# Kernel optimization log

Measured on AMD Instinct MI355X. Metric: run time of the kernel, lower is better.

The kernel has to match this reference:

```python
import jax, jax.numpy as jnp
import numpy as np

N_HEAD = 8
D_MODEL = 128  # per-head dim == d_model in this 'interpretable' MHA
B, S = 2, 2048
LN_EPS = 1e-3  # keras LayerNormalization default epsilon


def setup_inputs() -> dict:
    key = jax.random.key(0)
    ks = jax.random.split(key, 8)
    sc = 1.0 / np.sqrt(D_MODEL)
    q = jax.random.normal(ks[0], (B, S, D_MODEL), jnp.float32)
    k = jax.random.normal(ks[1], (B, S, D_MODEL), jnp.float32)
    v = jax.random.normal(ks[2], (B, S, D_MODEL), jnp.float32)
    # multiplicative causal mask (lower-triangular ones), broadcast over B,H
    mask = jnp.tril(jnp.ones((S, S), jnp.float32))[None, None, :, :]
    Wq = jax.random.normal(ks[3], (D_MODEL, N_HEAD * D_MODEL), jnp.float32) * sc
    Wk = jax.random.normal(ks[4], (D_MODEL, N_HEAD * D_MODEL), jnp.float32) * sc
    Wv = jax.random.normal(ks[5], (D_MODEL, N_HEAD * D_MODEL), jnp.float32) * sc
    Wo = jax.random.normal(ks[6], (N_HEAD * D_MODEL, D_MODEL), jnp.float32) * sc
    gamma = jnp.ones((D_MODEL,), jnp.float32)
    beta = jnp.zeros((D_MODEL,), jnp.float32)
    return {"q": q, "k": k, "v": v, "mask": mask, "Wq": Wq, "Wk": Wk,
            "Wv": Wv, "Wo": Wo, "gamma": gamma, "beta": beta}


def reference(q, k, v, mask, Wq, Wk, Wv, Wo, gamma, beta):
    b = q.shape[0]
    # projections -> [B, H, S, D]
    def split_heads(x):
        return x.reshape(b, -1, N_HEAD, D_MODEL).transpose(0, 2, 1, 3)
    qs = split_heads(q @ Wq)
    ks_ = split_heads(k @ Wk)
    vs = split_heads(v @ Wv)
    scores = jnp.einsum('bhqd,bhkd->bhqk', qs, ks_) / jnp.sqrt(jnp.float32(D_MODEL))
    scores = scores * mask  # multiplicative mask (NOT additive -inf)
    attn = jax.nn.softmax(scores, axis=-1)
    # dropout layers are identity at inference
    out = jnp.einsum('bhqk,bhkd->bhqd', attn, vs)
    out = out.transpose(0, 2, 1, 3).reshape(b, -1, N_HEAD * D_MODEL)
    out = out @ Wo
    # keras LayerNorm (axis=-1, eps=1e-3)
    mu = jnp.mean(out, axis=-1, keepdims=True)
    var = jnp.var(out, axis=-1, keepdims=True)
    out = (out - mu) * jax.lax.rsqrt(var + LN_EPS) * gamma + beta
    return out
```

## Files before the change

### kernel.cpp

```cpp
#include <hip/hip_runtime.h>
#include <math.h>

#define B 2
#define S 2048
#define H 8
#define D 128
#define DM 1024
#define BH 16

typedef unsigned short u16;
typedef __attribute__((ext_vector_type(8))) short bf16x8;
typedef __attribute__((ext_vector_type(8))) unsigned short u16x8;
typedef __attribute__((ext_vector_type(4))) float f32x4;

__device__ __forceinline__ float bf2f(u16 x) {
    union { unsigned u; float f; } c; c.u = ((unsigned)x) << 16; return c.f;
}
__device__ __forceinline__ u16 f2bf(float f) {
    union { unsigned u; float f; } c; c.f = f;
    unsigned u = c.u; u += 0x7fffu + ((u >> 16) & 1u);
    return (u16)(u >> 16);
}
__device__ __forceinline__ u16 ftr(float f) {
    union { unsigned u; float f; } c; c.f = f;
    return (u16)(c.u >> 16);
}

#define MFMA16(a, b, c) __builtin_amdgcn_mfma_f32_16x16x32_bf16((a), (b), (c), 0, 0, 0)

__device__ __forceinline__ void gload_lds16(const void* g, void* l) {
    __builtin_amdgcn_global_load_lds(
        (__attribute__((address_space(1))) void*)(unsigned long long)(g),
        (__attribute__((address_space(3))) void*)(unsigned long long)(l), 16, 0, 0);
}

__global__ __launch_bounds__(256) void prep_kernel(
    const float* __restrict__ Wq, const float* __restrict__ Wk, const float* __restrict__ Wv,
    const float* __restrict__ Wo, u16* __restrict__ WT, u16* __restrict__ WoT)
{
    __shared__ __align__(16) u16 Wl[128][132];
    int tid = threadIdx.x, by = blockIdx.x;
    if (by < 16) {
        int k0 = by * 64;
#pragma unroll
        for (int i = 0; i < 8; i++) {
            int e = i * 256 + tid; int kk = e >> 5, n4 = e & 31;
            float4 w4 = *(const float4*)&Wo[(size_t)(k0 + kk) * D + n4 * 4];
            ushort4 p; p.x = ftr(w4.x); p.y = ftr(w4.y); p.z = ftr(w4.z); p.w = ftr(w4.w);
            *(ushort4*)&Wl[kk][n4 * 4] = p;
        }
        __syncthreads();
#pragma unroll
        for (int i = 0; i < 4; i++) {
            int e = i * 256 + tid; int n = e >> 3, ko = e & 7;
            u16x8 g;
#pragma unroll
            for (int j = 0; j < 8; j++) g[j] = Wl[ko * 8 + j][n];
            *(u16x8*)&WoT[(size_t)n * DM + k0 + ko * 8] = g;
        }
    } else {
        int tile = by - 16;
        int t = tile >> 3, h = tile & 7;
        const float* W = (t == 0) ? Wq : (t == 1) ? Wk : Wv;
        int col0 = h * 128;
#pragma unroll
        for (int i = 0; i < 16; i++) {
            int e = i * 256 + tid; int kk = e >> 5, n4 = e & 31;
            float4 w4 = *(const float4*)&W[(size_t)kk * DM + col0 + n4 * 4];
            ushort4 p; p.x = ftr(w4.x); p.y = ftr(w4.y); p.z = ftr(w4.z); p.w = ftr(w4.w);
            *(ushort4*)&Wl[kk][n4 * 4] = p;
        }
        __syncthreads();
        u16* WTt = WT + (size_t)tile * (128 * 128);
#pragma unroll
        for (int i = 0; i < 8; i++) {
            int e = i * 256 + tid; int n = e >> 4, ko = e & 15;
            u16x8 g;
#pragma unroll
            for (int j = 0; j < 8; j++) g[j] = Wl[ko * 8 + j][n];
            *(u16x8*)&WTt[(size_t)n * 128 + ko * 8] = g;
        }
    }
}

__global__ __launch_bounds__(256) void proj_kernel(
    const float* __restrict__ q, const float* __restrict__ k, const float* __restrict__ v,
    const u16* __restrict__ WT,
    u16* __restrict__ Qo, u16* __restrict__ Ko, u16* __restrict__ VTo,
    float* __restrict__ Csum)
{
    __shared__ __align__(16) u16 Xs[64][136];
    __shared__ __align__(16) u16 Ws[128][136];
    int tid = threadIdx.x;
    int m0 = blockIdx.x * 64;
    int by = blockIdx.y;
    int t = by >> 3;
    int h = by & 7;
    const float* X = (t == 0) ? q : (t == 1) ? k : v;
    const u16* WTt = WT + (size_t)(t * 8 + h) * (128 * 128);

#pragma unroll
    for (int i = 0; i < 8; i++) {
        int e = i * 256 + tid; int r = e >> 5, c4 = e & 31;
        float4 x4 = *(const float4*)&X[(size_t)(m0 + r) * D + c4 * 4];
        ushort4 p; p.x = ftr(x4.x); p.y = ftr(x4.y); p.z = ftr(x4.z); p.w = ftr(x4.w);
        *(ushort4*)&Xs[r][c4 * 4] = p;
    }
#pragma unroll
    for (int i = 0; i < 8; i++) {
        int e = i * 256 + tid; int n = e >> 4, c8 = e & 15;
        *(u16x8*)&Ws[n][c8 * 8] = *(const u16x8*)&WTt[(size_t)n * 128 + c8 * 8];
    }
    __syncthreads();

    int w = tid >> 6, lane = tid & 63, quad = lane >> 4, ln = lane & 15;
    bf16x8 aX[4];
#pragma unroll
    for (int ks = 0; ks < 4; ks++)
        aX[ks] = *(const bf16x8*)&Xs[w * 16 + ln][ks * 32 + quad * 8];

    f32x4 zero = {0.f, 0.f, 0.f, 0.f};
    f32x4 acc[8];
#pragma unroll
    for (int nt = 0; nt < 8; nt++) acc[nt] = zero;

#pragma unroll
    for (int ks = 0; ks < 4; ks++) {
        bf16x8 bW[8];
#pragma unroll
        for (int nt = 0; nt < 8; nt++)
            bW[nt] = *(const bf16x8*)&Ws[nt * 16 + ln][ks * 32 + quad * 8];
#pragma unroll
        for (int nt = 0; nt < 8; nt++)
            acc[nt] = MFMA16(aX[ks], bW[nt], acc[nt]);
    }

    int bb = m0 >> 11, ss0 = m0 & 2047;
    int bh = bb * 8 + h;
    __syncthreads();
    if (t < 2) {
        u16 (*Ct)[136] = Xs;
        u16* O = (t == 0) ? Qo : Ko;
#pragma unroll
        for (int nt = 0; nt < 8; nt++)
#pragma unroll
            for (int r = 0; r < 4; r++)
                Ct[w * 16 + quad * 4 + r][nt * 16 + ln] = f2bf(acc[nt][r]);
        __syncthreads();
#pragma unroll
        for (int i = 0; i < 4; i++) {
            int e = i * 256 + tid; int r = e >> 4, c8 = e & 15;
            *(u16x8*)&O[((size_t)bh * S + ss0 + r) * D + c8 * 8] = *(const u16x8*)&Ct[r][c8 * 8];
        }
    } else {
        u16 (*Ct)[68] = (u16 (*)[68])&Xs[0][0];
#pragma unroll
        for (int nt = 0; nt < 8; nt++)
#pragma unroll
            for (int r = 0; r < 4; r++)
                Ct[nt * 16 + ln][w * 16 + quad * 4 + r] = f2bf(acc[nt][r]);
        __syncthreads();
#pragma unroll
        for (int i = 0; i < 4; i++) {
            int e = i * 256 + tid; int dloc = e >> 3, c8 = e & 7;
            *(u16x8*)&VTo[((size_t)bh * D + dloc) * S + ss0 + c8 * 8] =
                *(const u16x8*)&Ct[dloc][c8 * 8];
        }
        if (tid < 128) {
            int d = tid;
            float s = 0.f;
#pragma unroll
            for (int i = 0; i < 8; i++) {
                u16x8 v8 = *(const u16x8*)&Ct[d][i * 8];
#pragma unroll
                for (int j = 0; j < 8; j++) s += bf2f(v8[j]);
            }
            Csum[((size_t)bh * 32 + (ss0 >> 6)) * D + d] = s;
        }
    }
}

__global__ __launch_bounds__(256, 2) void attn_kernel(
    const u16* __restrict__ Qb, const u16* __restrict__ Kb, const u16* __restrict__ VTg,
    const float* __restrict__ Csum, u16* __restrict__ HOb)
{
    __shared__ __align__(16) u16 Ks[2][64][128];
    __shared__ __align__(16) u16 Vt[128][64];
    __shared__ __align__(16) u16 Ps[64][68];
    __shared__ float Lred[4][64];

    int tid = threadIdx.x;
    int bh = blockIdx.x;
    int y  = blockIdx.y;
    int qb = 31 - y;
    int q0 = qb * 64;
    int ntile = qb + 1;
    int w = tid >> 6, lane = tid & 63, quad = lane >> 4, ln = lane & 15;
    const u16* Qp  = Qb  + (size_t)bh * S * D;
    const u16* Kp  = Kb  + (size_t)bh * S * D;
    const u16* VTp = VTg + (size_t)bh * D * S;

#pragma unroll
    for (int i = 0; i < 4; i++) {
        int ci = i * 256 + tid;
        int r = ci >> 4, c = ci & 15;
        int sc = c ^ (r & 7);
        gload_lds16(&Qp[(size_t)(q0 + r) * D + sc * 8], (u16*)&Ks[1][0][0] + ci * 8);
    }
#pragma unroll
    for (int i = 0; i < 4; i++) {
        int ci = i * 256 + tid;
        int r = ci >> 4, c = ci & 15;
        int sc = c ^ (r & 7);
        gload_lds16(&Kp[(size_t)r * D + sc * 8], (u16*)&Ks[0][0][0] + ci * 8);
    }
    asm volatile("s_waitcnt vmcnt(4)" ::: "memory");
    __builtin_amdgcn_sched_barrier(0);
    __builtin_amdgcn_s_barrier();
    bf16x8 aQ[4][4];
#pragma unroll
    for (int rf = 0; rf < 4; rf++)
#pragma unroll
        for (int ks = 0; ks < 4; ks++) {
            int R = rf * 16 + ln;
            aQ[rf][ks] = *(const bf16x8*)&Ks[1][R][((ks * 4 + quad) ^ (R & 7)) * 8];
        }
    asm volatile("s_waitcnt vmcnt(0) lgkmcnt(0)" ::: "memory");
    __builtin_amdgcn_sched_barrier(0);
    __builtin_amdgcn_s_barrier();
#pragma unroll
    for (int i = 0; i < 4; i++) {
        int ci = i * 256 + tid;
        int dd = ci >> 3, c = ci & 7;
        int sc = c ^ (dd & 7);
        gload_lds16(&VTp[(size_t)dd * S + sc * 8], (u16*)&Vt[0][0] + ci * 8);
    }

    f32x4 zero = {0.f, 0.f, 0.f, 0.f};
    f32x4 accPV[4][2], acc_l[4];
#pragma unroll
    for (int rf = 0; rf < 4; rf++) { accPV[rf][0] = zero; accPV[rf][1] = zero; acc_l[rf] = zero; }
    bf16x8 bOnes;
#pragma unroll
    for (int j = 0; j < 8; j++) bOnes[j] = (short)0x3F80;
    const float scale = 0.08838834764831845f;

    for (int kt = 0; kt < ntile; kt++) {
        int cur = kt & 1, nxt = cur ^ 1;
        int k0 = kt * 64;
        bool pf = (kt + 1 < ntile);
        if (pf) {
#pragma unroll
            for (int i = 0; i < 4; i++) {
                int ci = i * 256 + tid;
                int r = ci >> 4, c = ci & 15;
                int sc = c ^ (r & 7);
                gload_lds16(&Kp[(size_t)(k0 + 64 + r) * D + sc * 8],
                            (u16*)&Ks[nxt][0][0] + ci * 8);
            }
        }
        f32x4 s[4];
#pragma unroll
        for (int rf = 0; rf < 4; rf++) s[rf] = zero;
        __builtin_amdgcn_s_setprio(1);
#pragma unroll
        for (int ks = 0; ks < 4; ks++) {
            int R = w * 16 + ln;
            bf16x8 bK = *(const bf16x8*)&Ks[cur][R][((ks * 4 + quad) ^ (R & 7)) * 8];
#pragma unroll
            for (int rf = 0; rf < 4; rf++)
                s[rf] = MFMA16(aQ[rf][ks], bK, s[rf]);
        }
        __builtin_amdgcn_s_setprio(0);
        int colb = k0 + w * 16 + ln;
#pragma unroll
        for (int rf = 0; rf < 4; rf++) {
            int rowb = q0 + rf * 16 + quad * 4;
#pragma unroll
            for (int r = 0; r < 4; r++) {
                float tv = (colb <= rowb + r) ? s[rf][r] : 0.f;
                Ps[rf * 16 + quad * 4 + r][w * 16 + ln] = f2bf(__expf(tv * scale));
            }
        }
        if (pf) asm volatile("s_waitcnt vmcnt(4) lgkmcnt(0)" ::: "memory");
        else    asm volatile("s_waitcnt vmcnt(0) lgkmcnt(0)" ::: "memory");
        __builtin_amdgcn_sched_barrier(0);
        __builtin_amdgcn_s_barrier();
        __builtin_amdgcn_s_setprio(1);
#pragma unroll
        for (int ks = 0; ks < 2; ks++) {
            bf16x8 aP[4];
#pragma unroll
            for (int rf = 0; rf < 4; rf++)
                aP[rf] = *(const bf16x8*)&Ps[rf * 16 + ln][ks * 32 + quad * 8];
            int rv0 = w * 32 + ln, rv1 = w * 32 + 16 + ln;
            bf16x8 v0 = *(const bf16x8*)&Vt[rv0][((ks * 4 + quad) ^ (rv0 & 7)) * 8];
            bf16x8 v1 = *(const bf16x8*)&Vt[rv1][((ks * 4 + quad) ^ (rv1 & 7)) * 8];
            if (((kt * 2 + ks) & 3) == w) {
#pragma unroll
                for (int rf = 0; rf < 4; rf++) acc_l[rf] = MFMA16(aP[rf], bOnes, acc_l[rf]);
            }
#pragma unroll
            for (int rf = 0; rf < 4; rf++) {
                accPV[rf][0] = MFMA16(aP[rf], v0, accPV[rf][0]);
                accPV[rf][1] = MFMA16(aP[rf], v1, accPV[rf][1]);
            }
        }
        __builtin_amdgcn_s_setprio(0);
        asm volatile("s_waitcnt vmcnt(0) lgkmcnt(0)" ::: "memory");
        __builtin_amdgcn_sched_barrier(0);
        __builtin_amdgcn_s_barrier();
        if (pf) {
#pragma unroll
            for (int i = 0; i < 4; i++) {
                int ci = i * 256 + tid;
                int dd = ci >> 3, c = ci & 7;
                int sc = c ^ (dd & 7);
                gload_lds16(&VTp[(size_t)dd * S + k0 + 64 + sc * 8], (u16*)&Vt[0][0] + ci * 8);
            }
        }
    }

    __syncthreads();
    if (ln == 0) {
#pragma unroll
        for (int rf = 0; rf < 4; rf++)
#pragma unroll
            for (int r = 0; r < 4; r++)
                Lred[w][rf * 16 + quad * 4 + r] = acc_l[rf][r];
    }
    __syncthreads();

    float suf0 = 0.f, suf1 = 0.f;
    for (int c = 31; c >= ntile; c--) {
        const float* cp = &Csum[((size_t)(bh * 32 + c)) * D + w * 32];
        suf0 += cp[ln];
        suf1 += cp[16 + ln];
    }
    int scount = S - ntile * 64;
    int b = bh >> 3, h = bh & 7;
#pragma unroll
    for (int rf = 0; rf < 4; rf++)
#pragma unroll
        for (int r = 0; r < 4; r++) {
            int row = rf * 16 + quad * 4 + r;
            int srow = q0 + row;
            float l = Lred[0][row] + Lred[1][row] + Lred[2][row] + Lred[3][row]
                      + (float)scount;
            float inv = 1.f / l;
            size_t base = ((size_t)(b * S + srow)) * DM + h * D + w * 32;
            HOb[base + ln]      = f2bf((accPV[rf][0][r] + suf0) * inv);
            HOb[base + 16 + ln] = f2bf((accPV[rf][1][r] + suf1) * inv);
        }
}

__global__ __launch_bounds__(256) void out_ln_kernel(
    const u16* __restrict__ HOb, const u16* __restrict__ WoT,
    const float* __restrict__ gamma, const float* __restrict__ beta,
    float* __restrict__ out)
{
    __shared__ __align__(16) u16 HOs[16][1048];
    __shared__ float Cs[16][132];
    int tid = threadIdx.x;
    int m0 = blockIdx.x * 16;
    int w = tid >> 6, lane = tid & 63, quad = lane >> 4, ln = lane & 15;
#pragma unroll
    for (int i = 0; i < 8; i++) {
        int e = i * 256 + tid; int r = e >> 7, c8 = e & 127;
        *(u16x8*)&HOs[r][c8 * 8] = *(const u16x8*)&HOb[(size_t)(m0 + r) * DM + c8 * 8];
    }
    __syncthreads();
    f32x4 zero = {0.f, 0.f, 0.f, 0.f};
    f32x4 acc[2] = {zero, zero};
#pragma unroll 4
    for (int ks = 0; ks < 32; ks++) {
        bf16x8 aH = *(const bf16x8*)&HOs[ln][ks * 32 + quad * 8];
        bf16x8 w0 = *(const bf16x8*)&WoT[(size_t)(w * 32 + ln) * DM + ks * 32 + quad * 8];
        bf16x8 w1 = *(const bf16x8*)&WoT[(size_t)(w * 32 + 16 + ln) * DM + ks * 32 + quad * 8];
        acc[0] = MFMA16(aH, w0, acc[0]);
        acc[1] = MFMA16(aH, w1, acc[1]);
    }
#pragma unroll
    for (int ct = 0; ct < 2; ct++)
#pragma unroll
        for (int r = 0; r < 4; r++)
            Cs[quad * 4 + r][w * 32 + ct * 16 + ln] = acc[ct][r];
    __syncthreads();

    int row = tid >> 4, t16 = tid & 15;
    float xv[8], sum = 0.f, sq = 0.f;
#pragma unroll
    for (int j = 0; j < 8; j++) {
        float x = Cs[row][t16 * 8 + j];
        xv[j] = x; sum += x; sq += x * x;
    }
#pragma unroll
    for (int off = 1; off < 16; off <<= 1) {
        sum += __shfl_xor(sum, off);
        sq  += __shfl_xor(sq, off);
    }
    float mu = sum * (1.f / 128.f);
    float var = sq * (1.f / 128.f) - mu * mu;
    float rstd = rsqrtf(var + 1e-3f);
    float o[8];
#pragma unroll
    for (int j = 0; j < 8; j++) {
        int c = t16 * 8 + j;
        o[j] = (xv[j] - mu) * rstd * gamma[c] + beta[c];
    }
    float* op = &out[(size_t)(m0 + row) * D + t16 * 8];
    *(float4*)&op[0] = *(float4*)&o[0];
    *(float4*)&op[4] = *(float4*)&o[4];
}

extern "C" void kernel_launch(void* const* d_in, const int* in_sizes, int n_in,
                              void* d_out, int out_size, void* d_ws, size_t ws_size,
                              hipStream_t stream)
{
    const float* q     = (const float*)d_in[0];
    const float* k     = (const float*)d_in[1];
    const float* v     = (const float*)d_in[2];
    const float* Wq    = (const float*)d_in[4];
    const float* Wk    = (const float*)d_in[5];
    const float* Wv    = (const float*)d_in[6];
    const float* Wo    = (const float*)d_in[7];
    const float* gamma = (const float*)d_in[8];
    const float* beta  = (const float*)d_in[9];

    u16* ws16 = (u16*)d_ws;
    u16* Qb  = ws16;
    u16* Kb  = ws16 + 4194304;
    u16* VT  = ws16 + 8388608;
    u16* HOb = ws16 + 12582912;
    u16* WoT = ws16 + 16777216;
    u16* WT  = ws16 + 16908288;
    float* Csum = (float*)((char*)d_ws + 35651584);

    prep_kernel<<<40, 256, 0, stream>>>(Wq, Wk, Wv, Wo, WT, WoT);
    proj_kernel<<<dim3(64, 24), 256, 0, stream>>>(q, k, v, WT, Qb, Kb, VT, Csum);
    attn_kernel<<<dim3(BH, 32), 256, 0, stream>>>(Qb, Kb, VT, Csum, HOb);
    out_ln_kernel<<<256, 256, 0, stream>>>(HOb, WoT, gamma, beta, (float*)d_out);
}
```

Baseline: 154.8 us.

## Pair causal query blocks per workgroup and widen attention tiles to 128 keys

The attention kernel now runs 512-thread workgroups, and each one handles two 64-row query blocks, j and 31-j, one after the other. Every workgroup therefore does the same 17 key-tile iterations, which removes the triangular load imbalance of the causal mask. Key and value tiles grow to 128 rows, V loading moves up front into the prologue, and the second query block is prefetched into a dedicated Q buffer. In exchange, shared memory per block and register pressure go up, and two in-loop epilogues add synchronization points.

```diff
diff --git a/kernel.cpp b/kernel.cpp
--- a/kernel.cpp
+++ b/kernel.cpp
@@ -33,6 +33,8 @@
         (__attribute__((address_space(1))) void*)(unsigned long long)(g),
         (__attribute__((address_space(3))) void*)(unsigned long long)(l), 16, 0, 0);
 }
+
+#define SWZ(R, CC) ((((CC) ^ ((R) & 7)) * 8))
 
 __global__ __launch_bounds__(256) void prep_kernel(
     const float* __restrict__ Wq, const float* __restrict__ Wk, const float* __restrict__ Wv,
@@ -180,41 +182,50 @@
     }
 }
 
-__global__ __launch_bounds__(256, 2) void attn_kernel(
+__global__ __launch_bounds__(512, 2) void attn_kernel(
     const u16* __restrict__ Qb, const u16* __restrict__ Kb, const u16* __restrict__ VTg,
     const float* __restrict__ Csum, u16* __restrict__ HOb)
 {
-    __shared__ __align__(16) u16 Ks[2][64][128];
-    __shared__ __align__(16) u16 Vt[128][64];
-    __shared__ __align__(16) u16 Ps[64][68];
+    __shared__ __align__(16) u16 Ks[2][128][128];
+    __shared__ __align__(16) u16 Vt[128][128];
+    __shared__ __align__(16) u16 Qs[64][128];
+    __shared__ __align__(16) u16 Ps[64][132];
     __shared__ float Lred[4][64];
 
     int tid = threadIdx.x;
     int bh = blockIdx.x;
-    int y  = blockIdx.y;
-    int qb = 31 - y;
-    int q0 = qb * 64;
-    int ntile = qb + 1;
+    int j  = blockIdx.y;
+    int qbA = 31 - j, qbB = j;
+    int nA = (qbA >> 1) + 1;
+    int nB = (qbB >> 1) + 1;
     int w = tid >> 6, lane = tid & 63, quad = lane >> 4, ln = lane & 15;
+    int bb = bh >> 3, hh = bh & 7;
     const u16* Qp  = Qb  + (size_t)bh * S * D;
     const u16* Kp  = Kb  + (size_t)bh * S * D;
     const u16* VTp = VTg + (size_t)bh * D * S;
 
 #pragma unroll
-    for (int i = 0; i < 4; i++) {
-        int ci = i * 256 + tid;
+    for (int i = 0; i < 2; i++) {
+        int ci = i * 512 + tid;
         int r = ci >> 4, c = ci & 15;
         int sc = c ^ (r & 7);
-        gload_lds16(&Qp[(size_t)(q0 + r) * D + sc * 8], (u16*)&Ks[1][0][0] + ci * 8);
+        gload_lds16(&Qp[(size_t)(qbA * 64 + r) * D + sc * 8], (u16*)&Qs[0][0] + ci * 8);
     }
 #pragma unroll
     for (int i = 0; i < 4; i++) {
-        int ci = i * 256 + tid;
+        int ci = i * 512 + tid;
         int r = ci >> 4, c = ci & 15;
         int sc = c ^ (r & 7);
         gload_lds16(&Kp[(size_t)r * D + sc * 8], (u16*)&Ks[0][0][0] + ci * 8);
     }
-    asm volatile("s_waitcnt vmcnt(4)" ::: "memory");
+#pragma unroll
+    for (int i = 0; i < 4; i++) {
+        int ci = i * 512 + tid;
+        int dd = ci >> 4, c = ci & 15;
+        int sc = c ^ (dd & 7);
+        gload_lds16(&VTp[(size_t)dd * S + sc * 8], (u16*)&Vt[0][0] + ci * 8);
+    }
+    asm volatile("s_waitcnt vmcnt(8)" ::: "memory");
     __builtin_amdgcn_sched_barrier(0);
     __builtin_amdgcn_s_barrier();
     bf16x8 aQ[4][4];
@@ -223,40 +234,74 @@
 #pragma unroll
         for (int ks = 0; ks < 4; ks++) {
             int R = rf * 16 + ln;
-            aQ[rf][ks] = *(const bf16x8*)&Ks[1][R][((ks * 4 + quad) ^ (R & 7)) * 8];
-        }
-    asm volatile("s_waitcnt vmcnt(0) lgkmcnt(0)" ::: "memory");
+            aQ[rf][ks] = *(const bf16x8*)&Qs[R][SWZ(R, ks * 4 + quad)];
+        }
+    asm volatile("s_waitcnt vmcnt(4) lgkmcnt(0)" ::: "memory");
     __builtin_amdgcn_sched_barrier(0);
     __builtin_amdgcn_s_barrier();
-#pragma unroll
-    for (int i = 0; i < 4; i++) {
-        int ci = i * 256 + tid;
-        int dd = ci >> 3, c = ci & 7;
-        int sc = c ^ (dd & 7);
-        gload_lds16(&VTp[(size_t)dd * S + sc * 8], (u16*)&Vt[0][0] + ci * 8);
-    }
 
     f32x4 zero = {0.f, 0.f, 0.f, 0.f};
-    f32x4 accPV[4][2], acc_l[4];
-#pragma unroll
-    for (int rf = 0; rf < 4; rf++) { accPV[rf][0] = zero; accPV[rf][1] = zero; acc_l[rf] = zero; }
+    f32x4 accPV[4], acc_l[4];
+#pragma unroll
+    for (int rf = 0; rf < 4; rf++) { accPV[rf] = zero; acc_l[rf] = zero; }
     bf16x8 bOnes;
 #pragma unroll
-    for (int j = 0; j < 8; j++) bOnes[j] = (short)0x3F80;
+    for (int jj = 0; jj < 8; jj++) bOnes[jj] = (short)0x3F80;
     const float scale = 0.08838834764831845f;
 
-    for (int kt = 0; kt < ntile; kt++) {
-        int cur = kt & 1, nxt = cur ^ 1;
-        int k0 = kt * 64;
-        bool pf = (kt + 1 < ntile);
+#define SEG_EPILOGUE(Q0_, NT_) do {                                              \
+    if (w < 4 && ln == 0) {                                                      \
+        _Pragma("unroll") for (int rf = 0; rf < 4; rf++)                         \
+        _Pragma("unroll") for (int r = 0; r < 4; r++)                            \
+            Lred[w][rf * 16 + quad * 4 + r] = acc_l[rf][r];                      \
+    }                                                                            \
+    asm volatile("s_waitcnt lgkmcnt(0)" ::: "memory");                           \
+    __builtin_amdgcn_sched_barrier(0);                                           \
+    __builtin_amdgcn_s_barrier();                                                \
+    int nt64 = 2 * (NT_);                                                        \
+    float suf = 0.f;                                                             \
+    for (int c = 31; c >= nt64; c--)                                             \
+        suf += Csum[((size_t)(bh * 32 + c)) * D + w * 16 + ln];                  \
+    int scount = S - (NT_) * 128;                                                \
+    _Pragma("unroll") for (int rf = 0; rf < 4; rf++)                             \
+    _Pragma("unroll") for (int r = 0; r < 4; r++) {                              \
+        int row = rf * 16 + quad * 4 + r;                                        \
+        int srow = (Q0_) + row;                                                  \
+        float l = Lred[0][row] + Lred[1][row] + Lred[2][row] + Lred[3][row]      \
+                  + (float)scount;                                               \
+        float inv = 1.f / l;                                                     \
+        HOb[((size_t)(bb * S + srow)) * DM + hh * D + w * 16 + ln] =             \
+            f2bf((accPV[rf][r] + suf) * inv);                                    \
+    }                                                                            \
+} while (0)
+
+#pragma unroll 1
+    for (int u = 0; u < 17; u++) {
+        int segB = (u >= nA);
+        int kt = segB ? (u - nA) : u;
+        int q0 = (segB ? qbB : qbA) * 64;
+        int cur = u & 1, nxt = cur ^ 1;
+        bool pf = (u + 1 < 17);
         if (pf) {
+            int u1 = u + 1;
+            int kt1 = (u1 >= nA) ? (u1 - nA) : u1;
 #pragma unroll
             for (int i = 0; i < 4; i++) {
-                int ci = i * 256 + tid;
+                int ci = i * 512 + tid;
                 int r = ci >> 4, c = ci & 15;
                 int sc = c ^ (r & 7);
-                gload_lds16(&Kp[(size_t)(k0 + 64 + r) * D + sc * 8],
+                gload_lds16(&Kp[(size_t)(kt1 * 128 + r) * D + sc * 8],
                             (u16*)&Ks[nxt][0][0] + ci * 8);
+            }
+        }
+        if (u == 0) {
+#pragma unroll
+            for (int i = 0; i < 2; i++) {
+                int ci = i * 512 + tid;
+                int r = ci >> 4, c = ci & 15;
+                int sc = c ^ (r & 7);
+                gload_lds16(&Qp[(size_t)(qbB * 64 + r) * D + sc * 8],
+                            (u16*)&Qs[0][0] + ci * 8);
             }
         }
         f32x4 s[4];
@@ -266,13 +311,13 @@
 #pragma unroll
         for (int ks = 0; ks < 4; ks++) {
             int R = w * 16 + ln;
-            bf16x8 bK = *(const bf16x8*)&Ks[cur][R][((ks * 4 + quad) ^ (R & 7)) * 8];
+            bf16x8 bK = *(const bf16x8*)&Ks[cur][R][SWZ(R, ks * 4 + quad)];
 #pragma unroll
             for (int rf = 0; rf < 4; rf++)
                 s[rf] = MFMA16(aQ[rf][ks], bK, s[rf]);
         }
         __builtin_amdgcn_s_setprio(0);
-        int colb = k0 + w * 16 + ln;
+        int colb = kt * 128 + w * 16 + ln;
 #pragma unroll
         for (int rf = 0; rf < 4; rf++) {
             int rowb = q0 + rf * 16 + quad * 4;
@@ -282,76 +327,60 @@
                 Ps[rf * 16 + quad * 4 + r][w * 16 + ln] = f2bf(__expf(tv * scale));
             }
         }
-        if (pf) asm volatile("s_waitcnt vmcnt(4) lgkmcnt(0)" ::: "memory");
-        else    asm volatile("s_waitcnt vmcnt(0) lgkmcnt(0)" ::: "memory");
+        if (u == 0)  asm volatile("s_waitcnt vmcnt(6) lgkmcnt(0)" ::: "memory");
+        else if (pf) asm volatile("s_waitcnt vmcnt(4) lgkmcnt(0)" ::: "memory");
+        else         asm volatile("s_waitcnt vmcnt(0) lgkmcnt(0)" ::: "memory");
         __builtin_amdgcn_sched_barrier(0);
         __builtin_amdgcn_s_barrier();
         __builtin_amdgcn_s_setprio(1);
 #pragma unroll
-        for (int ks = 0; ks < 2; ks++) {
+        for (int ks = 0; ks < 4; ks++) {
             bf16x8 aP[4];
 #pragma unroll
             for (int rf = 0; rf < 4; rf++)
                 aP[rf] = *(const bf16x8*)&Ps[rf * 16 + ln][ks * 32 + quad * 8];
-            int rv0 = w * 32 + ln, rv1 = w * 32 + 16 + ln;
-            bf16x8 v0 = *(const bf16x8*)&Vt[rv0][((ks * 4 + quad) ^ (rv0 & 7)) * 8];
-            bf16x8 v1 = *(const bf16x8*)&Vt[rv1][((ks * 4 + quad) ^ (rv1 & 7)) * 8];
-            if (((kt * 2 + ks) & 3) == w) {
+            int Rv = w * 16 + ln;
+            bf16x8 vb = *(const bf16x8*)&Vt[Rv][SWZ(Rv, ks * 4 + quad)];
+            if (w < 4 && ks == w) {
 #pragma unroll
                 for (int rf = 0; rf < 4; rf++) acc_l[rf] = MFMA16(aP[rf], bOnes, acc_l[rf]);
             }
 #pragma unroll
-            for (int rf = 0; rf < 4; rf++) {
-                accPV[rf][0] = MFMA16(aP[rf], v0, accPV[rf][0]);
-                accPV[rf][1] = MFMA16(aP[rf], v1, accPV[rf][1]);
-            }
+            for (int rf = 0; rf < 4; rf++)
+                accPV[rf] = MFMA16(aP[rf], vb, accPV[rf]);
         }
         __builtin_amdgcn_s_setprio(0);
         asm volatile("s_waitcnt vmcnt(0) lgkmcnt(0)" ::: "memory");
         __builtin_amdgcn_sched_barrier(0);
         __builtin_amdgcn_s_barrier();
         if (pf) {
+            int u1 = u + 1;
+            int kt1 = (u1 >= nA) ? (u1 - nA) : u1;
 #pragma unroll
             for (int i = 0; i < 4; i++) {
-                int ci = i * 256 + tid;
-                int dd = ci >> 3, c = ci & 7;
+                int ci = i * 512 + tid;
+                int dd = ci >> 4, c = ci & 15;
                 int sc = c ^ (dd & 7);
-                gload_lds16(&VTp[(size_t)dd * S + k0 + 64 + sc * 8], (u16*)&Vt[0][0] + ci * 8);
-            }
-        }
-    }
-
-    __syncthreads();
-    if (ln == 0) {
-#pragma unroll
-        for (int rf = 0; rf < 4; rf++)
-#pragma unroll
-            for (int r = 0; r < 4; r++)
-                Lred[w][rf * 16 + quad * 4 + r] = acc_l[rf][r];
-    }
-    __syncthreads();
-
-    float suf0 = 0.f, suf1 = 0.f;
-    for (int c = 31; c >= ntile; c--) {
-        const float* cp = &Csum[((size_t)(bh * 32 + c)) * D + w * 32];
-        suf0 += cp[ln];
-        suf1 += cp[16 + ln];
-    }
-    int scount = S - ntile * 64;
-    int b = bh >> 3, h = bh & 7;
-#pragma unroll
-    for (int rf = 0; rf < 4; rf++)
-#pragma unroll
-        for (int r = 0; r < 4; r++) {
-            int row = rf * 16 + quad * 4 + r;
-            int srow = q0 + row;
-            float l = Lred[0][row] + Lred[1][row] + Lred[2][row] + Lred[3][row]
-                      + (float)scount;
-            float inv = 1.f / l;
-            size_t base = ((size_t)(b * S + srow)) * DM + h * D + w * 32;
-            HOb[base + ln]      = f2bf((accPV[rf][0][r] + suf0) * inv);
-            HOb[base + 16 + ln] = f2bf((accPV[rf][1][r] + suf1) * inv);
-        }
+                gload_lds16(&VTp[(size_t)dd * S + kt1 * 128 + sc * 8],
+                            (u16*)&Vt[0][0] + ci * 8);
+            }
+        }
+        if (u == nA - 1) {
+            SEG_EPILOGUE(qbA * 64, nA);
+#pragma unroll
+            for (int rf = 0; rf < 4; rf++) { accPV[rf] = zero; acc_l[rf] = zero; }
+#pragma unroll
+            for (int rf = 0; rf < 4; rf++)
+#pragma unroll
+                for (int ks = 0; ks < 4; ks++) {
+                    int R = rf * 16 + ln;
+                    aQ[rf][ks] = *(const bf16x8*)&Qs[R][SWZ(R, ks * 4 + quad)];
+                }
+        }
+    }
+
+    SEG_EPILOGUE(qbB * 64, nB);
+#undef SEG_EPILOGUE
 }
 
 __global__ __launch_bounds__(256) void out_ln_kernel(
@@ -438,6 +467,6 @@
 
     prep_kernel<<<40, 256, 0, stream>>>(Wq, Wk, Wv, Wo, WT, WoT);
     proj_kernel<<<dim3(64, 24), 256, 0, stream>>>(q, k, v, WT, Qb, Kb, VT, Csum);
-    attn_kernel<<<dim3(BH, 32), 256, 0, stream>>>(Qb, Kb, VT, Csum, HOb);
+    attn_kernel<<<dim3(BH, 16), 512, 0, stream>>>(Qb, Kb, VT, Csum, HOb);
     out_ln_kernel<<<256, 256, 0, stream>>>(HOb, WoT, gamma, beta, (float*)d_out);
 }
```

New measurement: 156.1 us. About the same (+0.8%).
